# Optimization experiments

Hardware: AMD Instinct MI355X
Metric: run time of the kernel (lower is better)

Reference implementation:

```python
import jax, jax.numpy as jnp
import numpy as np


def setup_inputs() -> dict:
    key = jax.random.key(0)
    k1, k2 = jax.random.split(key)
    N, L, Q, H, Lv, P = 1, 6, 300, 8, 4, 4
    # FPN levels for an 800x1333 image at strides 8/16/32/64 (H, W per level)
    spatial_shapes = np.array([[100, 167], [50, 84], [25, 42], [13, 21]], dtype=np.int64)
    level_start_index = np.concatenate([[0], np.cumsum(spatial_shapes.prod(1))[:-1]]).astype(np.int64)
    sampling_locations = jax.random.uniform(k1, (N, L, Q, H, Lv, P, 2), dtype=jnp.float32)
    # attention weights normalized over (levels*points) per head, as MSDeformAttn produces
    aw = jax.random.normal(k2, (N, L, Q, H, Lv, P), dtype=jnp.float32)
    attention_weights = jax.nn.softmax(aw.reshape(N, L, Q, H, Lv * P), axis=-1).reshape(N, L, Q, H, Lv, P)
    return dict(sampling_locations=sampling_locations,
                attention_weights=attention_weights,
                spatial_shapes=spatial_shapes,
                level_start_index=level_start_index)


def reference(sampling_locations, attention_weights, spatial_shapes, level_start_index):
    # sampling_locations: (N, L, Q, H, Lv, P, 2); attention_weights: (N, L, Q, H, Lv, P)
    N, L, Q, H, Lv, P, _ = sampling_locations.shape
    S = int(np.sum(np.asarray(spatial_shapes)[:, 0] * np.asarray(spatial_shapes)[:, 1]))  # static
    ss = jnp.asarray(spatial_shapes)          # (Lv, 2) = (H, W)
    lsi = jnp.asarray(level_start_index)      # (Lv,)

    # permute(0,1,3,2,5,4,6).flatten(0,3) -> (M, P, Lv, 2) with M = N*L*H*Q
    sl = jnp.transpose(sampling_locations, (0, 1, 3, 2, 5, 4, 6)).reshape(-1, P, Lv, 2)
    aw = jnp.transpose(attention_weights, (0, 1, 3, 2, 5, 4)).reshape(-1, P, Lv)
    M = aw.shape[0]

    rev = ss[:, ::-1].astype(sl.dtype)        # (Lv, 2) = (W, H)
    crf = sl * rev                            # float (col, row) coords, (M, P, Lv, 2)
    crll = jnp.floor(crf)
    f = crf - crll                            # fractional part, (M, P, Lv, 2)
    fc, fr = f[..., 0], f[..., 1]

    # corners (d_col, d_row) paired with their bilinear margins (matches torch zipped order)
    offsets = jnp.array([[0, 0], [0, 1], [1, 0], [1, 1]], dtype=jnp.int32)  # ll, lh, hl, hh
    margins = jnp.stack([(fc - 1.0) * (fr - 1.0),   # margin_hh for corner ll
                         -(fc - 1.0) * fr,           # margin_hl for corner lh
                         -fc * (fr - 1.0),           # margin_lh for corner hl
                         fc * fr], axis=0)           # margin_ll for corner hh  -> (4, M, P, Lv)

    cri = crll.astype(jnp.int32)[None] + offsets[:, None, None, None, :]    # (4, M, P, Lv, 2)
    Wlv = ss[:, 1].astype(jnp.int32)
    Hlv = ss[:, 0].astype(jnp.int32)
    valid = ((cri[..., 0] >= 0) & (cri[..., 0] < Wlv) &
             (cri[..., 1] >= 0) & (cri[..., 1] < Hlv))                       # (4, M, P, Lv)

    idx = (cri[..., 1] * Wlv + cri[..., 0] + lsi.astype(jnp.int32)) * valid  # invalid -> 0
    w = aw[None] * valid * margins                                           # invalid -> 0 weight

    # single fused scatter-add over all 4 corners
    idx_flat = jnp.moveaxis(idx, 0, 1).reshape(M, -1)   # (M, 4*P*Lv)
    w_flat = jnp.moveaxis(w, 0, 1).reshape(M, -1)
    rows = jnp.arange(M)[:, None]
    flat_grid = jnp.zeros((M, S), dtype=jnp.float32).at[rows, idx_flat].add(w_flat)

    # torch: reshape(N, Len_q, n_layers, n_heads, -1).sum((2,3)).permute(0,2,1)
    return jnp.transpose(flat_grid.reshape(N, Q, L, H, S).sum(axis=(2, 3)), (0, 2, 1))
```

## Files before the change

### kernel.cpp

```cpp
#include <hip/hip_runtime.h>


constexpr int NQ   = 300;
constexpr int QW   = 8;
constexpr int NG   = 38;
constexpr int NTILES = 21;
constexpr int MAXC = 1280;
constexpr int BLK  = 512;
constexpr int GSTRIDE = 24;

__global__ __launch_bounds__(BLK, 8)
void msda_tiled(const float4* __restrict__ loc4,
                const float4* __restrict__ aw4,
                float*        __restrict__ out) {
    __shared__ float sm[QW * MAXC];

    const int b  = blockIdx.x;
    const int g  = b / GSTRIDE;
    const int tb = b - g * GSTRIDE;
    if (tb >= NTILES) return;

    int lv, r0t, nr;
    if (tb < 15)      { lv = 0; r0t = 7  * tb;        nr = min(7,  100 - r0t); }
    else if (tb < 19) { lv = 1; r0t = 15 * (tb - 15); nr = min(15, 50  - r0t); }
    else if (tb < 20) { lv = 2; r0t = 0;              nr = 25; }
    else              { lv = 3; r0t = 0;              nr = 13; }

    const int Wlv_[4] = {167, 84, 42, 21};
    const int Hlv_[4] = {100, 50, 25, 13};
    const int lsi_[4] = {0, 16700, 20900, 21950};
    const int W    = Wlv_[lv];
    const int base = lsi_[lv];
    const int g0   = g * QW;
    const int qw   = min(QW, NQ - g0);
    const int cells = nr * W;
    const int tid  = threadIdx.x;

    const int nm  = 48 * qw;
    float4 xy01, xy23, w4;
    int ql = 0;
    if (tid < nm) {
        const int mi = tid;
        const int m  = 48 * g0 + mi;
        ql = mi / 48;
        const int l  = m / 2400;
        const int rem = m - l * 2400;
        const int h  = rem / 300;
        const int q  = rem - h * 300;
        const int t  = (((l * 300 + q) * 8 + h) * 4 + lv) * 4;
        xy01 = loc4[(t >> 1) + 0];
        xy23 = loc4[(t >> 1) + 1];
        w4   = aw4[t >> 2];
    }

    {
        const int nz = qw * (MAXC / 4);
        float4* sm4 = (float4*)sm;
        for (int i = tid; i < nz; i += BLK) sm4[i] = make_float4(0.f, 0.f, 0.f, 0.f);
    }
    __syncthreads();

    const int rlo = r0t, rhi = r0t + nr;
    const float fW = (float)W, fH = (float)Hlv_[lv];

    if (tid < nm) {
        float* smq = &sm[ql * MAXC];

        #pragma unroll
        for (int p = 0; p < 4; ++p) {
            const float x = (p == 0) ? xy01.x : (p == 1) ? xy01.z : (p == 2) ? xy23.x : xy23.z;
            const float y = (p == 0) ? xy01.y : (p == 1) ? xy01.w : (p == 2) ? xy23.y : xy23.w;
            const float w = (p == 0) ? w4.x   : (p == 1) ? w4.y   : (p == 2) ? w4.z   : w4.w;

            const float cf  = x * fW;
            const float rf  = y * fH;
            const float cfl = floorf(cf), rfl = floorf(rf);
            const float fc  = cf - cfl, fr = rf - rfl;
            const int c0 = (int)cfl, rr = (int)rfl;
            const int c1 = c0 + 1, r1 = rr + 1;

            const bool cv0 = (unsigned)c0 < (unsigned)W;
            const bool cv1 = (unsigned)c1 < (unsigned)W;
            const bool rv0 = (rr >= rlo) & (rr < rhi);
            const bool rv1 = (r1 >= rlo) & (r1 < rhi);

            const float omfc = 1.0f - fc, omfr = 1.0f - fr;
            if (rv0) {
                const int ro = (rr - rlo) * W;
                if (cv0) atomicAdd(&smq[ro + c0], w * omfc * omfr);
                if (cv1) atomicAdd(&smq[ro + c1], w * fc   * omfr);
            }
            if (rv1) {
                const int ro = (r1 - rlo) * W;
                if (cv0) atomicAdd(&smq[ro + c0], w * omfc * fr);
                if (cv1) atomicAdd(&smq[ro + c1], w * fc   * fr);
            }
        }
    }
    __syncthreads();

    const int s0  = base + r0t * W;
    const int nq4 = qw >> 2;
    for (int i = tid; i < cells * nq4; i += BLK) {
        const int cell = i / nq4;
        const int v    = i - cell * nq4;
        float4 val;
        val.x = sm[(v * 4 + 0) * MAXC + cell];
        val.y = sm[(v * 4 + 1) * MAXC + cell];
        val.z = sm[(v * 4 + 2) * MAXC + cell];
        val.w = sm[(v * 4 + 3) * MAXC + cell];
        *(float4*)&out[(s0 + cell) * NQ + g0 + v * 4] = val;
    }
}

extern "C" void kernel_launch(void* const* d_in, const int* in_sizes, int n_in,
                              void* d_out, int out_size, void* d_ws, size_t ws_size,
                              hipStream_t stream) {
    const float4* loc4 = (const float4*)d_in[0];
    const float4* aw4  = (const float4*)d_in[1];
    float* out = (float*)d_out;

    msda_tiled<<<NG * GSTRIDE, BLK, 0, stream>>>(loc4, aw4, out);
}
```

Measured before the change: 84.61 us.

## Add pre-pass compacting per-level sampling data into contiguous workspace

A new kernel regroups sampling locations and attention weights by level into a contiguous workspace. The main kernel then reads each thread's 48 bytes from consecutive addresses instead of the strided per-level slices of the original layout. The grid also drops the padded GSTRIDE of 24 and uses exactly 21 tiles per group, removing idle blocks. The trade-off is an extra kernel launch plus a full write and re-read of the staged data.

New measurement: 82.92 us. 2.0% less time.

```diff
diff --git a/kernel.cpp b/kernel.cpp
--- a/kernel.cpp
+++ b/kernel.cpp
@@ -7,18 +7,38 @@
 constexpr int NTILES = 21;
 constexpr int MAXC = 1280;
 constexpr int BLK  = 512;
-constexpr int GSTRIDE = 24;
+constexpr int MTOT = 14400;
+
+__global__ __launch_bounds__(256, 8)
+void msda_compact(const float4* __restrict__ loc4,
+                  const float4* __restrict__ aw4,
+                  float4*       __restrict__ ws4) {
+    const int tid = blockIdx.x * 256 + threadIdx.x;
+    if (tid >= MTOT * 4) return;
+    const int lv = tid & 3;
+    const int m  = tid >> 2;
+    const int l  = m / 2400;
+    const int rem = m - l * 2400;
+    const int h  = rem / 300;
+    const int q  = rem - h * 300;
+    const int s  = (l * 300 + q) * 8 + h;
+    const float4 a = loc4[8 * s + 2 * lv];
+    const float4 b = loc4[8 * s + 2 * lv + 1];
+    const float4 c = aw4[4 * s + lv];
+    float4* dst = &ws4[((size_t)(lv * MTOT + m)) * 3];
+    dst[0] = a;
+    dst[1] = b;
+    dst[2] = c;
+}
 
 __global__ __launch_bounds__(BLK, 8)
-void msda_tiled(const float4* __restrict__ loc4,
-                const float4* __restrict__ aw4,
+void msda_tiled(const float4* __restrict__ ws4,
                 float*        __restrict__ out) {
     __shared__ float sm[QW * MAXC];
 
     const int b  = blockIdx.x;
-    const int g  = b / GSTRIDE;
-    const int tb = b - g * GSTRIDE;
-    if (tb >= NTILES) return;
+    const int g  = b / NTILES;
+    const int tb = b % NTILES;
 
     int lv, r0t, nr;
     if (tb < 15)      { lv = 0; r0t = 7  * tb;        nr = min(7,  100 - r0t); }
@@ -41,16 +61,11 @@
     int ql = 0;
     if (tid < nm) {
         const int mi = tid;
-        const int m  = 48 * g0 + mi;
         ql = mi / 48;
-        const int l  = m / 2400;
-        const int rem = m - l * 2400;
-        const int h  = rem / 300;
-        const int q  = rem - h * 300;
-        const int t  = (((l * 300 + q) * 8 + h) * 4 + lv) * 4;
-        xy01 = loc4[(t >> 1) + 0];
-        xy23 = loc4[(t >> 1) + 1];
-        w4   = aw4[t >> 2];
+        const float4* src = &ws4[((size_t)(lv * MTOT + 48 * g0 + mi)) * 3];
+        xy01 = src[0];
+        xy23 = src[1];
+        w4   = src[2];
     }
 
     {
@@ -118,7 +133,9 @@
                               hipStream_t stream) {
     const float4* loc4 = (const float4*)d_in[0];
     const float4* aw4  = (const float4*)d_in[1];
-    float* out = (float*)d_out;
+    float* out  = (float*)d_out;
+    float4* ws4 = (float4*)d_ws;
 
-    msda_tiled<<<NG * GSTRIDE, BLK, 0, stream>>>(loc4, aw4, out);
+    msda_compact<<<(MTOT * 4) / 256, 256, 0, stream>>>(loc4, aw4, ws4);
+    msda_tiled<<<NG * NTILES, BLK, 0, stream>>>(ws4, out);
 }
```
